# Kernel optimization log

Hardware: AMD Instinct MI355X
Metric: run time of the kernel (lower is better)

## Reference

```python
import jax, jax.numpy as jnp
import numpy as np

D_MODEL, D_STATE, D_CONV, EXPAND = 1024, 16, 4, 2
D_INNER = EXPAND * D_MODEL
DT_RANK = (D_MODEL + 15) // 16  # 64
B_SZ, SEQ = 2, 1024


def _mamba_dir(x, inW, convW, convB, xpW, dtW, dtB, Alog, Dp, outW):
    """Standard Mamba block forward. x: [B, L, d_model]."""
    Bsz, L, _ = x.shape
    d_inner, d_state = Alog.shape
    dt_rank = xpW.shape[0] - 2 * d_state
    xz = jnp.einsum('bld,ed->ble', x, inW)            # [B, L, 2*d_inner]
    xi, z = jnp.split(xz, 2, axis=-1)
    # depthwise causal conv along L
    xc = jnp.swapaxes(xi, 1, 2)                       # [B, d_inner, L]
    xc = jax.lax.conv_general_dilated(
        xc, convW, window_strides=(1,),
        padding=[(convW.shape[-1] - 1, 0)],
        feature_group_count=d_inner)
    xc = xc + convB[None, :, None]
    u = jax.nn.silu(jnp.swapaxes(xc, 1, 2))           # [B, L, d_inner]
    x_dbl = jnp.einsum('bld,ed->ble', u, xpW)         # [B, L, dt_rank+2N]
    dt, Bm, Cm = jnp.split(x_dbl, [dt_rank, dt_rank + d_state], axis=-1)
    delta = jax.nn.softplus(jnp.einsum('blr,dr->bld', dt, dtW) + dtB)  # [B,L,d_inner]
    A = -jnp.exp(Alog)                                # [d_inner, d_state]

    def step(h, ins):
        d_t, B_t, C_t, u_t = ins                      # [B,D],[B,N],[B,N],[B,D]
        dA = jnp.exp(d_t[:, :, None] * A)             # [B, D, N]
        h = h * dA + (d_t * u_t)[:, :, None] * B_t[:, None, :]
        y_t = jnp.einsum('bdn,bn->bd', h, C_t)
        return h, y_t

    h0 = jnp.zeros((Bsz, d_inner, d_state), x.dtype)
    xs = (jnp.swapaxes(delta, 0, 1), jnp.swapaxes(Bm, 0, 1),
          jnp.swapaxes(Cm, 0, 1), jnp.swapaxes(u, 0, 1))
    _, ys = jax.lax.scan(step, h0, xs)
    y = jnp.swapaxes(ys, 0, 1)                        # [B, L, d_inner]
    y = y + u * Dp
    y = y * jax.nn.silu(z)
    return jnp.einsum('bld,od->blo', y, outW)         # [B, L, d_model]


def _make_params(key, suffix):
    ks = jax.random.split(key, 10)
    s = 0.02
    p = {
        'inW' + suffix: jax.random.normal(ks[0], (2 * D_INNER, D_MODEL), jnp.float32) * s,
        'convW' + suffix: jax.random.normal(ks[1], (D_INNER, 1, D_CONV), jnp.float32) * s,
        'convB' + suffix: jnp.zeros((D_INNER,), jnp.float32),
        'xpW' + suffix: jax.random.normal(ks[2], (DT_RANK + 2 * D_STATE, D_INNER), jnp.float32) * s,
        'dtW' + suffix: jax.random.normal(ks[3], (D_INNER, DT_RANK), jnp.float32) * s,
        'dtB' + suffix: jax.random.normal(ks[4], (D_INNER,), jnp.float32) * 0.1 - 4.0,
        'Alog' + suffix: jnp.log(1.0 + jax.random.uniform(ks[5], (D_INNER, D_STATE), jnp.float32) * 15.0),
        'Dp' + suffix: jnp.ones((D_INNER,), jnp.float32),
        'outW' + suffix: jax.random.normal(ks[6], (D_MODEL, D_INNER), jnp.float32) * s,
    }
    return p


def setup_inputs() -> dict:
    key = jax.random.key(0)
    kx, kf, kb = jax.random.split(key, 3)
    inp = {'x': jax.random.normal(kx, (B_SZ, SEQ, D_MODEL), jnp.float32)}
    inp.update(_make_params(kf, '_f'))
    inp.update(_make_params(kb, '_b'))
    return inp


def reference(x, inW_f, convW_f, convB_f, xpW_f, dtW_f, dtB_f, Alog_f, Dp_f, outW_f,
              inW_b, convW_b, convB_b, xpW_b, dtW_b, dtB_b, Alog_b, Dp_b, outW_b):
    y_fwd = _mamba_dir(x, inW_f, convW_f, convB_f, xpW_f, dtW_f, dtB_f, Alog_f, Dp_f, outW_f)
    xb = jnp.flip(x, axis=1)
    y_bwd = jnp.flip(_mamba_dir(xb, inW_b, convW_b, convB_b, xpW_b, dtW_b, dtB_b, Alog_b, Dp_b, outW_b), axis=1)
    return 0.5 * (y_fwd + y_bwd)
```

## Files before the change

### kernel.cpp

```cpp
#include <hip/hip_runtime.h>
#include <math.h>

#define B_SZ 2
#define SEQ  1024
#define DM   1024
#define DI   2048
#define NST  16
#define RNK  64
#define XPD  96
#define M_TOT (B_SZ*SEQ)
#define NC   64
#define LC   (SEQ/NC)
#define NCH  65536

typedef unsigned short ushort_t;
typedef __attribute__((ext_vector_type(8))) short short8;
typedef __attribute__((ext_vector_type(4))) float f32x4;

#if __has_builtin(__builtin_amdgcn_exp2f)
#define EXP2F __builtin_amdgcn_exp2f
#else
#define EXP2F exp2f
#endif
#define LOG2E 1.44269504f

__device__ __forceinline__ ushort_t f2bf(float f) {
    unsigned u = __float_as_uint(f);
    u += 0x7fff + ((u >> 16) & 1);
    return (ushort_t)(u >> 16);
}
__device__ __forceinline__ float bf2f(ushort_t v) {
    return __uint_as_float(((unsigned)v) << 16);
}

__global__ __launch_bounds__(256)
void convert_all(const float* __restrict__ x,
                 const float* __restrict__ inWf, const float* __restrict__ inWb,
                 const float* __restrict__ outWf, const float* __restrict__ outWb,
                 const float* __restrict__ xpWf, const float* __restrict__ xpWb,
                 ushort_t* __restrict__ xbf, ushort_t* __restrict__ inWcat,
                 ushort_t* __restrict__ outWcat, ushort_t* __restrict__ xpWcat)
{
    int bid = blockIdx.x;
    const float* src; ushort_t* dst; int rel; int strided = 0;
    if (bid < 2048)       { rel = bid;         src = x;     dst = xbf; }
    else if (bid < 6144)  { rel = bid - 2048;  src = inWf;  dst = inWcat; }
    else if (bid < 10240) { rel = bid - 6144;  src = inWb;  dst = inWcat + (size_t)2 * DI * DM; }
    else if (bid < 12288) { rel = bid - 10240; src = outWf; dst = outWcat;      strided = 1; }
    else if (bid < 14336) { rel = bid - 12288; src = outWb; dst = outWcat + DI; strided = 1; }
    else if (bid < 14528) { rel = bid - 14336; src = xpWf;  dst = xpWcat; }
    else                  { rel = bid - 14528; src = xpWb;  dst = xpWcat + (size_t)XPD * DI; }
    int i = rel * 256 + threadIdx.x;
    float4 v = ((const float4*)src)[i];
    ushort4 o;
    o.x = f2bf(v.x); o.y = f2bf(v.y); o.z = f2bf(v.z); o.w = f2bf(v.w);
    if (!strided) {
        ((ushort4*)dst)[i] = o;
    } else {
        int row = i >> 9;
        int c4  = (i - (row << 9)) << 2;
        *(ushort4*)(dst + (size_t)row * (2 * DI) + c4) = o;
    }
}

__device__ __forceinline__ void load_lds16(const ushort_t* g, ushort_t* l) {
    __builtin_amdgcn_global_load_lds(
        (const __attribute__((address_space(1))) void*)g,
        (__attribute__((address_space(3))) void*)l, 16, 0, 0);
}

__device__ __forceinline__ void stageHalf(const ushort_t* g, int grow0, int K, int kt,
                                          ushort_t* lds, int w8, int l8, int gch)
{
    const ushort_t* p = g + (size_t)(grow0 + w8 + l8) * K + (size_t)kt * 64 + (gch << 3);
    load_lds16(p,                  lds + w8 * 64);
    load_lds16(p + (size_t)64 * K, lds + (64 + w8) * 64);
}

__device__ __forceinline__ void rdA4(const ushort_t* buf, int rbase, int sw0, int sw1,
                                     short8 (&a)[4][2])
{
#pragma unroll
    for (int i = 0; i < 4; i++) {
        const ushort_t* p = buf + (size_t)(rbase + i * 16) * 64;
        a[i][0] = *(const short8*)(p + sw0);
        a[i][1] = *(const short8*)(p + sw1);
    }
}
__device__ __forceinline__ void rdB2(const ushort_t* buf, int rbase, int sw0, int sw1,
                                     short8 (&bb)[2][2])
{
#pragma unroll
    for (int j = 0; j < 2; j++) {
        const ushort_t* p = buf + (size_t)(rbase + j * 16) * 64;
        bb[j][0] = *(const short8*)(p + sw0);
        bb[j][1] = *(const short8*)(p + sw1);
    }
}
__device__ __forceinline__ void mm16(const short8 (&a)[4][2], const short8 (&bb)[2][2],
                                     f32x4 (&acc)[4][2])
{
#pragma unroll
    for (int i = 0; i < 4; i++)
#pragma unroll
        for (int j = 0; j < 2; j++) {
            acc[i][j] = __builtin_amdgcn_mfma_f32_16x16x32_bf16(a[i][0], bb[j][0], acc[i][j], 0, 0, 0);
            acc[i][j] = __builtin_amdgcn_mfma_f32_16x16x32_bf16(a[i][1], bb[j][1], acc[i][j], 0, 0, 0);
        }
}

#define BAR()        __builtin_amdgcn_s_barrier()
#define SCHEDB()     __builtin_amdgcn_sched_barrier(0)
#define PRIO1()      __builtin_amdgcn_s_setprio(1)
#define PRIO0()      __builtin_amdgcn_s_setprio(0)
#define WAIT_LGKM0() asm volatile("s_waitcnt lgkmcnt(0)" ::: "memory")
#define WAIT_VM6()   asm volatile("s_waitcnt vmcnt(6)"  ::: "memory")
#define WAIT_VM0()   asm volatile("s_waitcnt vmcnt(0)"  ::: "memory")

__global__ __launch_bounds__(512, 2)
void gemm256_bf16(const ushort_t* __restrict__ A, const ushort_t* __restrict__ W,
                  ushort_t* __restrict__ D, int K, int ldD)
{
    __shared__ __align__(16) ushort_t As[2][256 * 64];
    __shared__ __align__(16) ushort_t Bs[2][256 * 64];

    const int t_   = threadIdx.x;
    const int lane = t_ & 63;
    const int wave = t_ >> 6;
    const int wrq  = wave >> 2;
    const int wcq  = wave & 3;
    const int lm   = lane & 15;
    const int w8   = wave << 3;
    const int l8   = lane >> 3;
    const int gch  = (lane & 7) ^ l8;
    const int sw0  = (((lane >> 4)    ) ^ (lane & 7)) << 3;
    const int sw1  = (((lane >> 4) + 4) ^ (lane & 7)) << 3;

    const int m0 = blockIdx.y * 256;
    const int n0 = blockIdx.x * 256;
    const int NT = K >> 6;

    const int rA0 = wrq * 64 + lm, rA1 = 128 + rA0;
    const int rB0 = wcq * 32 + lm, rB1 = 128 + rB0;

    f32x4 acc[2][2][4][2] = {};
    short8 a[4][2], b0[2][2], b1[2][2];

    stageHalf(A, m0,       K, 0, &As[0][0],        w8, l8, gch);
    stageHalf(A, m0 + 128, K, 0, &As[0][128 * 64], w8, l8, gch);
    stageHalf(W, n0,       K, 0, &Bs[0][0],        w8, l8, gch);
    stageHalf(W, n0 + 128, K, 0, &Bs[0][128 * 64], w8, l8, gch);
    if (NT > 1) {
        stageHalf(A, m0,       K, 1, &As[1][0],        w8, l8, gch);
        stageHalf(W, n0,       K, 1, &Bs[1][0],        w8, l8, gch);
        stageHalf(W, n0 + 128, K, 1, &Bs[1][128 * 64], w8, l8, gch);
        WAIT_VM6();
    } else {
        WAIT_VM0();
    }
    BAR();

    for (int t = 0; t < NT; ++t) {
        const int b = t & 1;
        const ushort_t* Ab = &As[b][0];
        const ushort_t* Bb = &Bs[b][0];
        ushort_t* Abw = &As[b][0];
        ushort_t* Bbw = &Bs[b][0];
        ushort_t* Aow = &As[b ^ 1][0];

        rdA4(Ab, rA0, sw0, sw1, a);
        rdB2(Bb, rB0, sw0, sw1, b0);
        if (t + 1 < NT) stageHalf(A, m0 + 128, K, t + 1, Aow + 128 * 64, w8, l8, gch);
        SCHEDB(); BAR(); WAIT_LGKM0(); SCHEDB();
        PRIO1(); mm16(a, b0, acc[0][0]); PRIO0();
        SCHEDB(); BAR();

        rdB2(Bb, rB1, sw0, sw1, b1);
        if (t + 2 < NT) stageHalf(A, m0, K, t + 2, Abw, w8, l8, gch);
        SCHEDB(); BAR(); WAIT_LGKM0(); SCHEDB();
        PRIO1(); mm16(a, b1, acc[0][1]); PRIO0();
        SCHEDB(); BAR();

        rdA4(Ab, rA1, sw0, sw1, a);
        if (t + 2 < NT) stageHalf(W, n0, K, t + 2, Bbw, w8, l8, gch);
        SCHEDB(); BAR(); WAIT_LGKM0(); SCHEDB();
        PRIO1(); mm16(a, b1, acc[1][1]); PRIO0();
        SCHEDB(); BAR();

        if (t + 2 < NT) stageHalf(W, n0 + 128, K, t + 2, Bbw + 128 * 64, w8, l8, gch);
        SCHEDB(); BAR();
        PRIO1(); mm16(a, b0, acc[1][0]); PRIO0();
        SCHEDB();
        if (t < NT - 2) { WAIT_VM6(); } else { WAIT_VM0(); }
        BAR();
    }

#pragma unroll
    for (int ih = 0; ih < 2; ih++)
#pragma unroll
        for (int i = 0; i < 4; i++)
#pragma unroll
            for (int r = 0; r < 4; r++) {
                int m = m0 + ih * 128 + wrq * 64 + i * 16 + ((lane >> 4) << 2) + r;
#pragma unroll
                for (int jh = 0; jh < 2; jh++)
#pragma unroll
                    for (int j = 0; j < 2; j++) {
                        int n = n0 + jh * 128 + wcq * 32 + j * 16 + lm;
                        D[(size_t)m * ldD + n] = f2bf(acc[ih][jh][i][j][r]);
                    }
            }
}

template<bool OUT_BF16>
__global__ __launch_bounds__(256)
void gemm_gll(const ushort_t* __restrict__ A, const ushort_t* __restrict__ W,
              void* __restrict__ D, int M, int N, int K, int kLen, int ldD)
{
    __shared__ __align__(16) ushort_t As[128 * 64];
    __shared__ __align__(16) ushort_t Ws[128 * 64];
    const int t    = threadIdx.x;
    const int lane = t & 63;
    const int wave = t >> 6;
    const int wr   = (wave >> 1) * 64;
    const int wc   = (wave & 1) * 64;

    const int m0 = blockIdx.y * 128;
    const int n0 = blockIdx.x * 128;
    const int kStart = blockIdx.z * kLen;

    const int srow   = lane >> 3;
    const int gchunk = (lane & 7) ^ srow;

    f32x4 acc[4][4] = {};

    for (int k0 = kStart; k0 < kStart + kLen; k0 += 64) {
#pragma unroll
        for (int it = 0; it < 4; it++) {
            const int rb = wave * 32 + it * 8;
            load_lds16(A + (size_t)(m0 + rb + srow) * K + k0 + gchunk * 8,
                       As + rb * 64);
            load_lds16(W + (size_t)(n0 + rb + srow) * K + k0 + gchunk * 8,
                       Ws + rb * 64);
        }
        __syncthreads();
#pragma unroll
        for (int kk = 0; kk < 2; kk++) {
            const int kc = kk * 4 + (lane >> 4);
            short8 af[4], bf[4];
#pragma unroll
            for (int i = 0; i < 4; i++) {
                int r = wr + i * 16 + (lane & 15);
                af[i] = *(const short8*)(As + r * 64 + ((kc ^ (r & 7)) << 3));
            }
#pragma unroll
            for (int j = 0; j < 4; j++) {
                int r = wc + j * 16 + (lane & 15);
                bf[j] = *(const short8*)(Ws + r * 64 + ((kc ^ (r & 7)) << 3));
            }
#pragma unroll
            for (int i = 0; i < 4; i++)
#pragma unroll
                for (int j = 0; j < 4; j++)
                    acc[i][j] = __builtin_amdgcn_mfma_f32_16x16x32_bf16(
                        af[i], bf[j], acc[i][j], 0, 0, 0);
        }
        __syncthreads();
    }

    if (OUT_BF16) {
        ushort_t* Dp = (ushort_t*)D;
#pragma unroll
        for (int i = 0; i < 4; i++)
#pragma unroll
            for (int r = 0; r < 4; r++) {
                int m = m0 + wr + i * 16 + ((lane >> 4) << 2) + r;
#pragma unroll
                for (int j = 0; j < 4; j++) {
                    int n = n0 + wc + j * 16 + (lane & 15);
                    Dp[(size_t)m * ldD + n] = f2bf(acc[i][j][r]);
                }
            }
    } else {
        float* Dp = (float*)D + (size_t)blockIdx.z * M * ldD;
#pragma unroll
        for (int i = 0; i < 4; i++)
#pragma unroll
            for (int r = 0; r < 4; r++) {
                int m = m0 + wr + i * 16 + ((lane >> 4) << 2) + r;
#pragma unroll
                for (int j = 0; j < 4; j++) {
                    int n = n0 + wc + j * 16 + (lane & 15);
                    Dp[(size_t)m * ldD + n] = acc[i][j][r];
                }
            }
    }
}

__global__ __launch_bounds__(256)
void reduce4(const float* __restrict__ P, float* __restrict__ out)
{
    int i = blockIdx.x * 256 + threadIdx.x;
    const size_t S = (size_t)M_TOT * DM / 4;
    float4 a = ((const float4*)P)[i];
    float4 b = ((const float4*)P)[i + S];
    float4 c = ((const float4*)P)[i + 2 * S];
    float4 d = ((const float4*)P)[i + 3 * S];
    float4 o;
    o.x = 0.5f * (a.x + b.x + c.x + d.x);
    o.y = 0.5f * (a.y + b.y + c.y + d.y);
    o.z = 0.5f * (a.z + b.z + c.z + d.z);
    o.w = 0.5f * (a.w + b.w + c.w + d.w);
    ((float4*)out)[i] = o;
}

#define LDSP 72

__global__ __launch_bounds__(256)
void gemm2_splitk2(const ushort_t* __restrict__ ubf, const ushort_t* __restrict__ xpWcat,
                   float* __restrict__ P)
{
    const int dir = blockIdx.z >> 3;
    const int kz  = blockIdx.z & 7;
    const ushort_t* A = ubf + (size_t)dir * M_TOT * DI;
    const ushort_t* W = xpWcat + (size_t)dir * XPD * DI;
    const int K = DI, N = XPD;

    __shared__ __align__(16) ushort_t As[64 * LDSP];
    __shared__ __align__(16) ushort_t Ws[64 * LDSP];
    const int t    = threadIdx.x;
    const int lane = t & 63;
    const int wave = t >> 6;
    const int wr   = (wave >> 1) * 32;
    const int wc   = (wave & 1) * 32;

    f32x4 acc[2][2] = {};

    const int m0 = blockIdx.y * 64;
    const int n0 = blockIdx.x * 64;
    const int kStart = kz * (DI / 8);
    const int srow = t >> 3;
    const int scol = (t & 7) << 3;

    for (int k0 = kStart; k0 < kStart + DI / 8; k0 += 64) {
        {
            int r = srow;
            short8 v = *(const short8*)(A + (size_t)(m0 + r) * K + k0 + scol);
            *(short8*)(&As[r * LDSP + scol]) = v;
            int r2 = 32 + srow;
            short8 v2 = *(const short8*)(A + (size_t)(m0 + r2) * K + k0 + scol);
            *(short8*)(&As[r2 * LDSP + scol]) = v2;
            int wn = n0 + r;
            short8 wv = {};
            if (wn < N) wv = *(const short8*)(W + (size_t)wn * K + k0 + scol);
            *(short8*)(&Ws[r * LDSP + scol]) = wv;
            int wn2 = n0 + r2;
            short8 wv2 = {};
            if (wn2 < N) wv2 = *(const short8*)(W + (size_t)wn2 * K + k0 + scol);
            *(short8*)(&Ws[r2 * LDSP + scol]) = wv2;
        }
        __syncthreads();
#pragma unroll
        for (int kk = 0; kk < 2; kk++) {
            const int kcol = kk * 32 + ((lane >> 4) << 3);
            short8 af[2], bfr[2];
#pragma unroll
            for (int i = 0; i < 2; i++)
                af[i] = *(const short8*)(&As[(wr + i * 16 + (lane & 15)) * LDSP + kcol]);
#pragma unroll
            for (int j = 0; j < 2; j++)
                bfr[j] = *(const short8*)(&Ws[(wc + j * 16 + (lane & 15)) * LDSP + kcol]);
#pragma unroll
            for (int i = 0; i < 2; i++)
#pragma unroll
                for (int j = 0; j < 2; j++)
                    acc[i][j] = __builtin_amdgcn_mfma_f32_16x16x32_bf16(
                        af[i], bfr[j], acc[i][j], 0, 0, 0);
        }
        __syncthreads();
    }

    float* Pz = P + ((size_t)dir * 8 + kz) * M_TOT * XPD;
#pragma unroll
    for (int i = 0; i < 2; i++)
#pragma unroll
        for (int r = 0; r < 4; r++) {
            int m = m0 + wr + i * 16 + ((lane >> 4) << 2) + r;
#pragma unroll
            for (int j = 0; j < 2; j++) {
                int n = n0 + wc + j * 16 + (lane & 15);
                if (n < N) Pz[(size_t)m * XPD + n] = acc[i][j][r];
            }
        }
}

__global__ __launch_bounds__(256)
void xdbl_reduce2(const float* __restrict__ P, float* __restrict__ xdbl)
{
    int bid = blockIdx.x;
    int dir = bid >= 192;
    int i = (bid - dir * 192) * 256 + threadIdx.x;
    const size_t S = (size_t)M_TOT * XPD / 4;
    const float4* Pd = (const float4*)(P + (size_t)dir * 8 * M_TOT * XPD);
    float4 s = Pd[i];
#pragma unroll
    for (int z = 1; z < 8; z++) {
        float4 v = Pd[i + z * S];
        s.x += v.x; s.y += v.y; s.z += v.z; s.w += v.w;
    }
    ((float4*)(xdbl + (size_t)dir * M_TOT * XPD))[i] = s;
}

__global__ __launch_bounds__(256)
void delta_gemm2(const float* __restrict__ xdbl,
                 const float* __restrict__ dtWf, const float* __restrict__ dtWb,
                 const float* __restrict__ dtBf, const float* __restrict__ dtBb,
                 ushort_t* __restrict__ deltab)
{
    const int dir = blockIdx.z;
    const float* xd  = xdbl + (size_t)dir * M_TOT * XPD;
    const float* dtW = dir ? dtWb : dtWf;
    const float* dtB = dir ? dtBb : dtBf;
    ushort_t* delta  = deltab + (size_t)dir * M_TOT * DI;

    __shared__ __align__(16) ushort_t As[64 * LDSP];
    __shared__ __align__(16) ushort_t Ws[64 * LDSP];
    const int t    = threadIdx.x;
    const int lane = t & 63;
    const int wave = t >> 6;
    const int wr   = (wave >> 1) * 32;
    const int wc   = (wave & 1) * 32;

    const int m0 = blockIdx.y * 64;
    const int n0 = blockIdx.x * 64;
    const int srow = t >> 2;
    const int scol = (t & 3) << 4;

    {
        const float* ap = xd  + (size_t)(m0 + srow) * XPD + scol;
        const float* wp = dtW + (size_t)(n0 + srow) * RNK + scol;
        float4 a[4], w[4];
#pragma unroll
        for (int q = 0; q < 4; q++) { a[q] = ((const float4*)ap)[q]; w[q] = ((const float4*)wp)[q]; }
        __align__(16) ushort_t at[16], wt[16];
#pragma unroll
        for (int q = 0; q < 16; q++) {
            at[q] = f2bf(((const float*)a)[q]);
            wt[q] = f2bf(((const float*)w)[q]);
        }
        *(short8*)(&As[srow * LDSP + scol])     = *(const short8*)(at);
        *(short8*)(&As[srow * LDSP + scol + 8]) = *(const short8*)(at + 8);
        *(short8*)(&Ws[srow * LDSP + scol])     = *(const short8*)(wt);
        *(short8*)(&Ws[srow * LDSP + scol + 8]) = *(const short8*)(wt + 8);
    }
    __syncthreads();

    f32x4 acc[2][2] = {};
#pragma unroll
    for (int kk = 0; kk < 2; kk++) {
        const int kcol = kk * 32 + ((lane >> 4) << 3);
        short8 af[2], bfr[2];
#pragma unroll
        for (int i = 0; i < 2; i++)
            af[i] = *(const short8*)(&As[(wr + i * 16 + (lane & 15)) * LDSP + kcol]);
#pragma unroll
        for (int j = 0; j < 2; j++)
            bfr[j] = *(const short8*)(&Ws[(wc + j * 16 + (lane & 15)) * LDSP + kcol]);
#pragma unroll
        for (int i = 0; i < 2; i++)
#pragma unroll
            for (int j = 0; j < 2; j++)
                acc[i][j] = __builtin_amdgcn_mfma_f32_16x16x32_bf16(
                    af[i], bfr[j], acc[i][j], 0, 0, 0);
    }

#pragma unroll
    for (int j = 0; j < 2; j++) {
        int n = n0 + wc + j * 16 + (lane & 15);
        float bn = dtB[n];
#pragma unroll
        for (int i = 0; i < 2; i++) {
#pragma unroll
            for (int r = 0; r < 4; r++) {
                int m = m0 + wr + i * 16 + ((lane >> 4) << 2) + r;
                float v = acc[i][j][r] + bn;
                float sp = (v > 20.f) ? v : log1pf(__expf(v));
                delta[(size_t)m * DI + n] = f2bf(sp);
            }
        }
    }
}

__global__ __launch_bounds__(256)
void conv_silu2(const ushort_t* __restrict__ xzall,
                const float* __restrict__ convWf, const float* __restrict__ convWb,
                const float* __restrict__ convBf, const float* __restrict__ convBb,
                ushort_t* __restrict__ ubf)
{
    int bid = blockIdx.x;
    int dir = bid >> 12;
    int idx = (bid & 4095) * 256 + threadIdx.x;
    const float* convW = dir ? convWb : convWf;
    const float* convB = dir ? convBb : convBf;
    int di  = (idx & (DI / 4 - 1)) << 2;
    int m   = idx >> 9;
    int b   = m >> 10, l = m & (SEQ - 1);
    const ushort_t* xb = xzall + (size_t)b * SEQ * (4 * DI) + dir * (2 * DI) + di;

    float wv[4][4];
#pragma unroll
    for (int c = 0; c < 4; c++) {
        float4 w = *(const float4*)(convW + (di + c) * 4);
        wv[c][0] = w.x; wv[c][1] = w.y; wv[c][2] = w.z; wv[c][3] = w.w;
    }
    float4 cb = *(const float4*)(convB + di);
    float acc[4] = {cb.x, cb.y, cb.z, cb.w};
#pragma unroll
    for (int j = 0; j < 4; j++) {
        int srcl = dir ? (l + 3 - j) : (l - 3 + j);
        if ((unsigned)srcl < SEQ) {
            ushort4 xv = *(const ushort4*)(xb + (size_t)srcl * (4 * DI));
            acc[0] += wv[0][j] * bf2f(xv.x);
            acc[1] += wv[1][j] * bf2f(xv.y);
            acc[2] += wv[2][j] * bf2f(xv.z);
            acc[3] += wv[3][j] * bf2f(xv.w);
        }
    }
    ushort4 o;
    o.x = f2bf(acc[0] / (1.f + __expf(-acc[0])));
    o.y = f2bf(acc[1] / (1.f + __expf(-acc[1])));
    o.z = f2bf(acc[2] / (1.f + __expf(-acc[2])));
    o.w = f2bf(acc[3] / (1.f + __expf(-acc[3])));
    *(ushort4*)(ubf + (size_t)dir * M_TOT * DI + (size_t)m * DI + di) = o;
}

__global__ __launch_bounds__(256)
void scan_pass1_2(const ushort_t* __restrict__ deltab, const ushort_t* __restrict__ ubf,
                  const float* __restrict__ xdbl,
                  const float* __restrict__ Alogf, const float* __restrict__ Alogb,
                  ushort_t* __restrict__ Sb, float* __restrict__ SD)
{
    int tid = threadIdx.x, lane = tid & 63, wv = tid >> 6;
    int blk = blockIdx.x;
    int dir = blk >> 10;
    blk &= 1023;
    int dg = blk & 7;
    int bc = blk >> 3;
    int c  = bc & (NC - 1);
    int b  = bc >> 6;
    int d  = (dg * 4 + wv) * 64 + lane;
    int t0 = dir ? (SEQ - 1 - c * LC) : (c * LC);
    int rs = dir ? -1 : 1;

    const float* Alog = dir ? Alogb : Alogf;
    const ushort_t* dl_p = deltab + (size_t)dir * M_TOT * DI;
    const ushort_t* u_p  = ubf    + (size_t)dir * M_TOT * DI;
    const float*    xd   = xdbl   + (size_t)dir * M_TOT * XPD;
    ushort_t* Sbd = Sb + (size_t)dir * NC * NCH;
    float* SDd = SD + (size_t)dir * NC * B_SZ * DI;

    float ac2[NST];
#pragma unroll
    for (int q = 0; q < 4; q++) {
        float4 al = *(const float4*)(Alog + (size_t)d * NST + q * 4);
        ac2[q * 4 + 0] = -__expf(al.x) * LOG2E;
        ac2[q * 4 + 1] = -__expf(al.y) * LOG2E;
        ac2[q * 4 + 2] = -__expf(al.z) * LOG2E;
        ac2[q * 4 + 3] = -__expf(al.w) * LOG2E;
    }
    float h[NST];
#pragma unroll
    for (int n = 0; n < NST; n++) h[n] = 0.f;
    float sumD = 0.f;

#pragma unroll 4
    for (int l = 0; l < LC; l++) {
        int t = t0 + rs * l;
        size_t row = (size_t)b * SEQ + t;
        float dl = bf2f(dl_p[row * DI + d]);
        float uv = bf2f(u_p[row * DI + d]);
        const float* xr = xd + row * XPD + RNK;
        float4 Bv[4];
#pragma unroll
        for (int q = 0; q < 4; q++) Bv[q] = *(const float4*)(xr + q * 4);
        float dlu = dl * uv;
        sumD += dl;
#pragma unroll
        for (int n = 0; n < NST; n++) {
            float dA = EXP2F(dl * ac2[n]);
            h[n] = h[n] * dA + dlu * ((const float*)Bv)[n];
        }
    }

    size_t o = (size_t)c * NCH + ((size_t)b * DI + d) * NST;
#pragma unroll
    for (int q = 0; q < 4; q++) {
        ushort4 pk;
        pk.x = f2bf(h[q * 4 + 0]);
        pk.y = f2bf(h[q * 4 + 1]);
        pk.z = f2bf(h[q * 4 + 2]);
        pk.w = f2bf(h[q * 4 + 3]);
        *(ushort4*)(Sbd + o + q * 4) = pk;
    }
    SDd[(size_t)c * (B_SZ * DI) + b * DI + d] = sumD;
}

__global__ __launch_bounds__(256)
void scan_combine2(ushort_t* __restrict__ Sb, const float* __restrict__ SD,
                   const float* __restrict__ Alogf, const float* __restrict__ Alogb)
{
    int gid = blockIdx.x * 256 + threadIdx.x;
    int dir = gid >= NCH;
    int i = gid - dir * NCH;
    int n = i & 15;
    int d = (i >> 4) & (DI - 1);
    int b = i >> 15;
    const float* Alog = dir ? Alogb : Alogf;
    ushort_t* Sbd = Sb + (size_t)dir * NC * NCH;
    const float* SDd = SD + (size_t)dir * NC * B_SZ * DI;
    float ac2 = -__expf(Alog[(size_t)d * NST + n]) * LOG2E;
    float h = 0.f;
#pragma unroll
    for (int c = 0; c < NC; c++) {
        float s = bf2f(Sbd[(size_t)c * NCH + i]);
        float p = EXP2F(ac2 * SDd[(size_t)c * (B_SZ * DI) + b * DI + d]);
        Sbd[(size_t)c * NCH + i] = f2bf(h);
        h = s + p * h;
    }
}

__global__ __launch_bounds__(256)
void scan_pass2_2(const ushort_t* __restrict__ deltab, const ushort_t* __restrict__ ubf,
                  const float* __restrict__ xdbl, const ushort_t* __restrict__ xzall,
                  const float* __restrict__ Alogf, const float* __restrict__ Alogb,
                  const float* __restrict__ Dpf, const float* __restrict__ Dpb,
                  const ushort_t* __restrict__ Hinit, ushort_t* __restrict__ ybf)
{
    int tid = threadIdx.x, lane = tid & 63, wv = tid >> 6;
    int blk = blockIdx.x;
    int dir = blk >> 10;
    blk &= 1023;
    int dg = blk & 7;
    int bc = blk >> 3;
    int c  = bc & (NC - 1);
    int b  = bc >> 6;
    int d  = (dg * 4 + wv) * 64 + lane;
    int t0 = dir ? (SEQ - 1 - c * LC) : (c * LC);
    int rs = dir ? -1 : 1;

    const float* Alog = dir ? Alogb : Alogf;
    const float* Dpp  = dir ? Dpb : Dpf;
    const ushort_t* dl_p = deltab + (size_t)dir * M_TOT * DI;
    const ushort_t* u_p  = ubf    + (size_t)dir * M_TOT * DI;
    const float*    xd   = xdbl   + (size_t)dir * M_TOT * XPD;
    const ushort_t* Hin  = Hinit  + (size_t)dir * NC * NCH;

    float ac2[NST];
#pragma unroll
    for (int q = 0; q < 4; q++) {
        float4 al = *(const float4*)(Alog + (size_t)d * NST + q * 4);
        ac2[q * 4 + 0] = -__expf(al.x) * LOG2E;
        ac2[q * 4 + 1] = -__expf(al.y) * LOG2E;
        ac2[q * 4 + 2] = -__expf(al.z) * LOG2E;
        ac2[q * 4 + 3] = -__expf(al.w) * LOG2E;
    }
    float dp = Dpp[d];
    float h[NST];
    {
        size_t o = (size_t)c * NCH + ((size_t)b * DI + d) * NST;
#pragma unroll
        for (int q = 0; q < 4; q++) {
            ushort4 hv = *(const ushort4*)(Hin + o + q * 4);
            h[q*4]   = bf2f(hv.x);
            h[q*4+1] = bf2f(hv.y);
            h[q*4+2] = bf2f(hv.z);
            h[q*4+3] = bf2f(hv.w);
        }
    }

#pragma unroll 4
    for (int l = 0; l < LC; l++) {
        int t = t0 + rs * l;
        size_t row = (size_t)b * SEQ + t;
        float dl = bf2f(dl_p[row * DI + d]);
        float uv = bf2f(u_p[row * DI + d]);
        const float* xr = xd + row * XPD + RNK;
        float4 Bv[4], Cv[4];
#pragma unroll
        for (int q = 0; q < 4; q++) {
            Bv[q] = *(const float4*)(xr + q * 4);
            Cv[q] = *(const float4*)(xr + NST + q * 4);
        }
        float dlu = dl * uv;
        float y = 0.f;
#pragma unroll
        for (int n = 0; n < NST; n++) {
            float dA = EXP2F(dl * ac2[n]);
            h[n] = h[n] * dA + dlu * ((const float*)Bv)[n];
            y += h[n] * ((const float*)Cv)[n];
        }
        float z = bf2f(xzall[row * (4 * DI) + dir * (2 * DI) + DI + d]);
        float yv = (y + uv * dp) * (z / (1.f + __expf(-z)));
        ybf[row * (2 * DI) + dir * DI + d] = f2bf(yv);
    }
}

extern "C" void kernel_launch(void* const* d_in, const int* in_sizes, int n_in,
                              void* d_out, int out_size, void* d_ws, size_t ws_size,
                              hipStream_t stream)
{
    char* wsb = (char*)d_ws;

    ushort_t* xzall  = (ushort_t*)wsb;
    ushort_t* ybf    = (ushort_t*)(wsb + 33554432);
    ushort_t* inWcat = (ushort_t*)(wsb + 50331648);
    ushort_t* outWcat= (ushort_t*)(wsb + 67108864);
    ushort_t* xbf    = (ushort_t*)(wsb + 75497472);
    ushort_t* xpWcat = (ushort_t*)(wsb + 79691776);
    ushort_t* ubf    = (ushort_t*)(wsb + 80478208);
    ushort_t* deltab = (ushort_t*)(wsb + 97255424);
    float*    xdbl   = (float*)(wsb + 114032640);

    ushort_t* Sb   = (ushort_t*)inWcat;
    float* SD    = (float*)xbf;
    float* part2 = (float*)deltab;
    float* part4 = (float*)xzall;

    float* out = (float*)d_out;
    dim3 blk(256);

    convert_all<<<14720, blk, 0, stream>>>(
        (const float*)d_in[0], (const float*)d_in[1], (const float*)d_in[10],
        (const float*)d_in[9], (const float*)d_in[18],
        (const float*)d_in[4], (const float*)d_in[13],
        xbf, inWcat, outWcat, xpWcat);

    gemm256_bf16<<<dim3(8192 / 256, M_TOT / 256), dim3(512), 0, stream>>>(
        xbf, inWcat, xzall, DM, 8192);

    conv_silu2<<<8192, blk, 0, stream>>>(xzall,
        (const float*)d_in[2], (const float*)d_in[11],
        (const float*)d_in[3], (const float*)d_in[12], ubf);

    gemm2_splitk2<<<dim3(2, M_TOT / 64, 16), blk, 0, stream>>>(ubf, xpWcat, part2);

    xdbl_reduce2<<<384, blk, 0, stream>>>(part2, xdbl);

    delta_gemm2<<<dim3(DI / 64, M_TOT / 64, 2), blk, 0, stream>>>(
        xdbl, (const float*)d_in[5], (const float*)d_in[14],
        (const float*)d_in[6], (const float*)d_in[15], deltab);

    scan_pass1_2<<<2048, blk, 0, stream>>>(deltab, ubf, xdbl,
        (const float*)d_in[7], (const float*)d_in[16], Sb, SD);
    scan_combine2<<<2 * NCH / 256, blk, 0, stream>>>(Sb, SD,
        (const float*)d_in[7], (const float*)d_in[16]);
    scan_pass2_2<<<2048, blk, 0, stream>>>(deltab, ubf, xdbl, xzall,
        (const float*)d_in[7], (const float*)d_in[16],
        (const float*)d_in[8], (const float*)d_in[17], Sb, ybf);

    gemm_gll<false><<<dim3(DM / 128, M_TOT / 128, 4), blk, 0, stream>>>(
        ybf, outWcat, part4, M_TOT, DM, 2 * DI, DI / 2, DM);

    reduce4<<<(M_TOT * DM / 4) / 256, blk, 0, stream>>>(part4, out);
}
```

Measured before the change: 338.8 us.

## Software-pipeline LDS fragment reads one phase ahead in bf16 GEMM main loop

Restructures the 256x256 GEMM main loop so that LDS fragment reads for the next MFMA phase, and for the next K-tile, are issued before the current phase's MFMAs. It uses partial lgkmcnt waits (4/8) instead of full drains, and spreads vmcnt waits across the phases. The goal is to hide LDS read latency behind MFMA work. The cost is an extra A fragment register set, which adds register pressure at 512 threads with 2 blocks per CU. The finer-grained wait counts also risk subtle correctness issues if the counts are miscounted.

```diff
diff --git a/kernel.cpp b/kernel.cpp
--- a/kernel.cpp
+++ b/kernel.cpp
@@ -77,22 +77,22 @@
     load_lds16(p + (size_t)64 * K, lds + (64 + w8) * 64);
 }
 
-__device__ __forceinline__ void rdA4(const ushort_t* buf, int rbase, int sw0, int sw1,
+__device__ __forceinline__ void rdA4(const ushort_t* half, int rbase, int sw0, int sw1,
                                      short8 (&a)[4][2])
 {
 #pragma unroll
     for (int i = 0; i < 4; i++) {
-        const ushort_t* p = buf + (size_t)(rbase + i * 16) * 64;
+        const ushort_t* p = half + (size_t)(rbase + i * 16) * 64;
         a[i][0] = *(const short8*)(p + sw0);
         a[i][1] = *(const short8*)(p + sw1);
     }
 }
-__device__ __forceinline__ void rdB2(const ushort_t* buf, int rbase, int sw0, int sw1,
+__device__ __forceinline__ void rdB2(const ushort_t* half, int rbase, int sw0, int sw1,
                                      short8 (&bb)[2][2])
 {
 #pragma unroll
     for (int j = 0; j < 2; j++) {
-        const ushort_t* p = buf + (size_t)(rbase + j * 16) * 64;
+        const ushort_t* p = half + (size_t)(rbase + j * 16) * 64;
         bb[j][0] = *(const short8*)(p + sw0);
         bb[j][1] = *(const short8*)(p + sw1);
     }
@@ -114,7 +114,9 @@
 #define PRIO1()      __builtin_amdgcn_s_setprio(1)
 #define PRIO0()      __builtin_amdgcn_s_setprio(0)
 #define WAIT_LGKM0() asm volatile("s_waitcnt lgkmcnt(0)" ::: "memory")
-#define WAIT_VM6()   asm volatile("s_waitcnt vmcnt(6)"  ::: "memory")
+#define WAIT_LGKM4() asm volatile("s_waitcnt lgkmcnt(4)" ::: "memory")
+#define WAIT_LGKM8() asm volatile("s_waitcnt lgkmcnt(8)" ::: "memory")
+#define WAIT_VM8()   asm volatile("s_waitcnt vmcnt(8)"  ::: "memory")
 #define WAIT_VM0()   asm volatile("s_waitcnt vmcnt(0)"  ::: "memory")
 
 __global__ __launch_bounds__(512, 2)
@@ -140,59 +142,70 @@
     const int n0 = blockIdx.x * 256;
     const int NT = K >> 6;
 
-    const int rA0 = wrq * 64 + lm, rA1 = 128 + rA0;
-    const int rB0 = wcq * 32 + lm, rB1 = 128 + rB0;
+    const int rA0 = wrq * 64 + lm;
+    const int rB0 = wcq * 32 + lm;
 
     f32x4 acc[2][2][4][2] = {};
-    short8 a[4][2], b0[2][2], b1[2][2];
+    short8 a0[4][2], a1[4][2], b0[2][2], b1[2][2];
 
     stageHalf(A, m0,       K, 0, &As[0][0],        w8, l8, gch);
-    stageHalf(A, m0 + 128, K, 0, &As[0][128 * 64], w8, l8, gch);
     stageHalf(W, n0,       K, 0, &Bs[0][0],        w8, l8, gch);
     stageHalf(W, n0 + 128, K, 0, &Bs[0][128 * 64], w8, l8, gch);
+    stageHalf(A, m0 + 128, K, 0, &As[0][128 * 64], w8, l8, gch);
     if (NT > 1) {
         stageHalf(A, m0,       K, 1, &As[1][0],        w8, l8, gch);
         stageHalf(W, n0,       K, 1, &Bs[1][0],        w8, l8, gch);
         stageHalf(W, n0 + 128, K, 1, &Bs[1][128 * 64], w8, l8, gch);
-        WAIT_VM6();
+        WAIT_VM8();
     } else {
         WAIT_VM0();
     }
+    SCHEDB();
     BAR();
+    rdA4(&As[0][0], rA0, sw0, sw1, a0);
+    rdB2(&Bs[0][0], rB0, sw0, sw1, b0);
 
     for (int t = 0; t < NT; ++t) {
         const int b = t & 1;
-        const ushort_t* Ab = &As[b][0];
-        const ushort_t* Bb = &Bs[b][0];
-        ushort_t* Abw = &As[b][0];
-        ushort_t* Bbw = &Bs[b][0];
-        ushort_t* Aow = &As[b ^ 1][0];
-
-        rdA4(Ab, rA0, sw0, sw1, a);
-        rdB2(Bb, rB0, sw0, sw1, b0);
-        if (t + 1 < NT) stageHalf(A, m0 + 128, K, t + 1, Aow + 128 * 64, w8, l8, gch);
-        SCHEDB(); BAR(); WAIT_LGKM0(); SCHEDB();
-        PRIO1(); mm16(a, b0, acc[0][0]); PRIO0();
+        const ushort_t* Ac = &As[b][0];
+        const ushort_t* Bc = &Bs[b][0];
+        const ushort_t* An = &As[b ^ 1][0];
+        const ushort_t* Bn = &Bs[b ^ 1][0];
+        ushort_t* Acw = &As[b][0];
+        ushort_t* Bcw = &Bs[b][0];
+        ushort_t* Anw = &As[b ^ 1][0];
+
+        if (t + 1 < NT) stageHalf(A, m0 + 128, K, t + 1, Anw + 128 * 64, w8, l8, gch);
+        WAIT_VM8();
+        rdB2(Bc + 128 * 64, rB0, sw0, sw1, b1);
+        SCHEDB(); BAR(); WAIT_LGKM4(); SCHEDB();
+        PRIO1(); mm16(a0, b0, acc[0][0]); PRIO0();
         SCHEDB(); BAR();
 
-        rdB2(Bb, rB1, sw0, sw1, b1);
-        if (t + 2 < NT) stageHalf(A, m0, K, t + 2, Abw, w8, l8, gch);
-        SCHEDB(); BAR(); WAIT_LGKM0(); SCHEDB();
-        PRIO1(); mm16(a, b1, acc[0][1]); PRIO0();
+        if (t + 2 < NT) stageHalf(A, m0, K, t + 2, Acw, w8, l8, gch);
+        WAIT_VM8();
+        rdA4(Ac + 128 * 64, rA0, sw0, sw1, a1);
+        SCHEDB(); BAR(); WAIT_LGKM8(); SCHEDB();
+        PRIO1(); mm16(a0, b1, acc[0][1]); PRIO0();
         SCHEDB(); BAR();
 
-        rdA4(Ab, rA1, sw0, sw1, a);
-        if (t + 2 < NT) stageHalf(W, n0, K, t + 2, Bbw, w8, l8, gch);
-        SCHEDB(); BAR(); WAIT_LGKM0(); SCHEDB();
-        PRIO1(); mm16(a, b1, acc[1][1]); PRIO0();
+        if (t + 2 < NT) stageHalf(W, n0, K, t + 2, Bcw, w8, l8, gch);
+        WAIT_VM8();
+        if (t + 1 < NT) {
+            rdA4(An, rA0, sw0, sw1, a0);
+            SCHEDB(); BAR(); WAIT_LGKM8(); SCHEDB();
+        } else {
+            SCHEDB(); BAR(); WAIT_LGKM0(); SCHEDB();
+        }
+        PRIO1(); mm16(a1, b0, acc[1][0]); PRIO0();
         SCHEDB(); BAR();
 
-        if (t + 2 < NT) stageHalf(W, n0 + 128, K, t + 2, Bbw + 128 * 64, w8, l8, gch);
+        if (t + 2 < NT) stageHalf(W, n0 + 128, K, t + 2, Bcw + 128 * 64, w8, l8, gch);
+        WAIT_VM8();
+        if (t + 1 < NT) rdB2(Bn, rB0, sw0, sw1, b0);
+        SCHEDB(); BAR(); SCHEDB();
+        PRIO1(); mm16(a1, b1, acc[1][1]); PRIO0();
         SCHEDB(); BAR();
-        PRIO1(); mm16(a, b0, acc[1][0]); PRIO0();
-        SCHEDB();
-        if (t < NT - 2) { WAIT_VM6(); } else { WAIT_VM0(); }
-        BAR();
     }
 
 #pragma unroll
```

Measured after the change: 353.2 us. 4.2% more time.
